# Kernel tuning notes

Measured on AMD Instinct MI355X. Metric: run time of the kernel, lower is better.

## Reference

```python
import jax, jax.numpy as jnp
import numpy as np
from jax.ops import segment_sum, segment_min, segment_max

N, E = 25000, 400000
NF, EF = 30, 10
H = 40          # n_hidden (multiple of towers)
T = 5           # towers
F = H           # F_in per tower (divide_input=False)
FO = H // T     # F_out per tower
L = 2           # gnn layers
NC = 2          # classes
EPS_BN = 1e-5


def setup_inputs() -> dict:
    key = jax.random.key(0)
    ks = jax.random.split(key, 24)
    r = lambda k, s, sc=0.1: jax.random.normal(k, s, jnp.float32) * sc
    return {
        "x": jax.random.normal(ks[0], (N, NF), jnp.float32),
        "edge_attr": jax.random.normal(ks[1], (E, EF), jnp.float32),
        "edge_index": jax.random.randint(ks[2], (2, E), 0, N, jnp.int32),
        "node_w": r(ks[3], (NF, H)), "node_b": r(ks[4], (H,)),
        "edge_w": r(ks[5], (EF, H)), "edge_b": r(ks[6], (H,)),
        "enc_w": r(ks[7], (L, H, F)), "enc_b": r(ks[8], (L, F)),
        "pre_w": r(ks[9], (L, T, 3 * F, F)), "pre_b": r(ks[10], (L, T, F)),
        "post_w": r(ks[11], (L, T, 13 * F, FO)), "post_b": r(ks[12], (L, T, FO)),
        "lin_w": r(ks[13], (L, H, H)), "lin_b": r(ks[14], (L, H)),
        "bn_g": jnp.ones((L, H), jnp.float32), "bn_b": jnp.zeros((L, H), jnp.float32),
        "mlp1_w": r(ks[15], (3 * H, 50)), "mlp1_b": r(ks[16], (50,)),
        "mlp2_w": r(ks[17], (50, 25)), "mlp2_b": r(ks[18], (25,)),
        "mlp3_w": r(ks[19], (25, NC)), "mlp3_b": r(ks[20], (NC,)),
    }


def _pna_conv(x, src, dst, e_emb, enc_w, enc_b, pre_w, pre_b, post_w, post_b,
              lin_w, lin_b, cnt, cnt1, amp, att):
    # message: per-tower pre-MLP on cat(x_i=dst, x_j=src, enc(edge_attr))
    e = e_emb @ enc_w + enc_b                                    # [E, F]
    h = jnp.concatenate([x[dst], x[src], e], axis=-1)            # [E, 3F]
    hs = jnp.einsum('ef,tfo->eto', h, pre_w) + pre_b             # [E, T, F]
    # multi-aggregation over incoming edges (index = dst)
    c = cnt1[:, None, None]
    mean = segment_sum(hs, dst, num_segments=N) / c
    msq = segment_sum(hs * hs, dst, num_segments=N) / c
    std = jnp.sqrt(jax.nn.relu(msq - mean * mean) + 1e-5)
    has = (cnt > 0)[:, None, None]
    mn = jnp.where(has, segment_min(hs, dst, num_segments=N), 0.0)
    mx = jnp.where(has, segment_max(hs, dst, num_segments=N), 0.0)
    agg = jnp.concatenate([mean, mn, mx, std], axis=-1)          # [N, T, 4F]
    agg = jnp.concatenate([agg, agg * amp, agg * att], axis=-1)  # [N, T, 12F]
    out = jnp.concatenate(
        [jnp.broadcast_to(x[:, None, :], (N, T, F)), agg], axis=-1)  # [N, T, 13F]
    out = jnp.einsum('ntf,tfo->nto', out, post_w) + post_b       # [N, T, FO]
    return out.reshape(N, T * FO) @ lin_w + lin_b                # [N, H]


def reference(x, edge_attr, node_w, node_b, edge_w, edge_b, enc_w, enc_b,
              pre_w, pre_b, post_w, post_b, lin_w, lin_b, bn_g, bn_b,
              mlp1_w, mlp1_b, mlp2_w, mlp2_b, mlp3_w, mlp3_b, edge_index):
    src, dst = edge_index[0], edge_index[1]
    cnt = segment_sum(jnp.ones((E,), jnp.float32), dst, num_segments=N)  # in-degree
    cnt1 = jnp.maximum(cnt, 1.0)                                 # deg.clamp_(1)
    log_deg = jnp.log(cnt1 + 1.0)
    avg_log = jnp.mean(jnp.log(cnt + 1.0))                       # PNA avg_deg['log']
    amp = (log_deg / avg_log)[:, None, None]
    att = (avg_log / log_deg)[:, None, None]
    h = x @ node_w + node_b                                      # node embedding
    e_emb = edge_attr @ edge_w + edge_b                          # edge embedding
    for i in range(L):
        c = _pna_conv(h, src, dst, e_emb, enc_w[i], enc_b[i], pre_w[i], pre_b[i],
                      post_w[i], post_b[i], lin_w[i], lin_b[i], cnt, cnt1, amp, att)
        mu = jnp.mean(c, axis=0)
        var = jnp.mean((c - mu) ** 2, axis=0)                    # BatchNorm (batch stats)
        cbn = (c - mu) / jnp.sqrt(var + EPS_BN) * bn_g[i] + bn_b[i]
        h = (h + jax.nn.relu(cbn)) / 2.0
    z = jax.nn.relu(jnp.concatenate([h[src], h[dst]], axis=-1))  # [E, 2H]
    z = jnp.concatenate([z, e_emb], axis=-1)                     # [E, 3H]
    z = jax.nn.relu(z @ mlp1_w + mlp1_b)
    z = jax.nn.relu(z @ mlp2_w + mlp2_b)
    return z @ mlp3_w + mlp3_b                                   # [E, NC]
```

## Files before the change

### kernel.cpp

```cpp
#include <hip/hip_runtime.h>
#include <hip/hip_bf16.h>
#include <cstdint>
#include <cstddef>

#define NN 25000
#define NE 400000
#define NFD 30
#define EFD 10
#define H 40
#define T 5
#define FO 8
#define LAYERS 2
#define TF 200
#define PSTR 52
#define REC 12
#define WCN 416
#define WCK 64
#define SHP 72
#define EPSV 1e-5f

typedef __attribute__((ext_vector_type(8))) short bf16x8;
typedef __attribute__((ext_vector_type(4))) float f32x4;

__device__ inline short bfbits(float v) {
    __hip_bfloat16 b = __float2bfloat16(v);
    return *(short*)&b;
}

__global__ __launch_bounds__(256) void k_deg(const int* __restrict__ dst, int* __restrict__ cnt) {
    int e = blockIdx.x * 256 + threadIdx.x;
    if (e < NE) atomicAdd(&cnt[dst[e]], 1);
}

__global__ __launch_bounds__(256) void k_avglog(const int* __restrict__ cnt, float* __restrict__ slot) {
    __shared__ float red[256];
    float s = 0.0f;
    for (int i = blockIdx.x * 256 + threadIdx.x; i < NN; i += gridDim.x * 256)
        s += logf((float)cnt[i] + 1.0f);
    red[threadIdx.x] = s; __syncthreads();
    for (int o = 128; o > 0; o >>= 1) {
        if (threadIdx.x < o) red[threadIdx.x] += red[threadIdx.x + o];
        __syncthreads();
    }
    if (threadIdx.x == 0) atomicAdd(slot, red[0]);
}

__global__ __launch_bounds__(256) void k_node(const float* __restrict__ x, const float* __restrict__ w,
                                              const float* __restrict__ b, float* __restrict__ h,
                                              const int* __restrict__ cnt, const float* __restrict__ slot,
                                              float* __restrict__ amp, float* __restrict__ att) {
    int id = blockIdx.x * 256 + threadIdx.x;
    if (id < NN) {
        float avg = slot[0] / (float)NN;
        float c1 = fmaxf((float)cnt[id], 1.0f);
        float lg = logf(c1 + 1.0f);
        amp[id] = lg / avg;
        att[id] = avg / lg;
    }
    if (id >= NN * H) return;
    int n = id / H, j = id - n * H;
    const float* xr = x + (size_t)n * NFD;
    float acc = b[j];
    #pragma unroll
    for (int m = 0; m < NFD; m++) acc += xr[m] * w[m * H + j];
    h[id] = acc;
}

__global__ __launch_bounds__(1024) void k_scan(const int* __restrict__ cnt, int* __restrict__ offs) {
    __shared__ int wsum[16];
    int tid = threadIdx.x;
    int lane = tid & 63, wv = tid >> 6;
    int runbase = 0;
    for (int base = 0; base < NN; base += 4096) {
        int i0 = base + tid * 4;
        int4 v = make_int4(0, 0, 0, 0);
        if (i0 < NN) v = *(const int4*)(cnt + i0);
        int tsum = v.x + v.y + v.z + v.w;
        int x = tsum;
        #pragma unroll
        for (int o = 1; o < 64; o <<= 1) {
            int y = __shfl_up(x, o);
            if (lane >= o) x += y;
        }
        if (lane == 63) wsum[wv] = x;
        __syncthreads();
        if (wv == 0 && lane < 16) {
            int wsv = wsum[lane];
            #pragma unroll
            for (int o = 1; o < 16; o <<= 1) {
                int y = __shfl_up(wsv, o);
                if (lane >= o) wsv += y;
            }
            wsum[lane] = wsv;
        }
        __syncthreads();
        int wpref = (wv > 0) ? wsum[wv - 1] : 0;
        int excl = runbase + wpref + x - tsum;
        if (i0 < NN) {
            offs[i0]     = excl;
            offs[i0 + 1] = excl + v.x;
            offs[i0 + 2] = excl + v.x + v.y;
            offs[i0 + 3] = excl + v.x + v.y + v.z;
        }
        runbase += wsum[15];
        __syncthreads();
    }
    if (tid == 0) offs[NN] = runbase;
}

__global__ __launch_bounds__(256) void k_scatter(const int* __restrict__ src, const int* __restrict__ dst,
                                                 const float* __restrict__ edge_attr,
                                                 const int* __restrict__ offs, int* __restrict__ fill,
                                                 float* __restrict__ ea_csr, int* __restrict__ pdst) {
    int e = blockIdx.x * 256 + threadIdx.x;
    if (e >= NE) return;
    int d = dst[e];
    int p = offs[d] + atomicAdd(&fill[d], 1);
    const float2* ear = (const float2*)(edge_attr + (size_t)e * EFD);
    float2 v0 = ear[0], v1 = ear[1], v2 = ear[2], v3 = ear[3], v4 = ear[4];
    float4* o = (float4*)(ea_csr + (size_t)p * REC);
    o[0] = make_float4(v0.x, v0.y, v1.x, v1.y);
    o[1] = make_float4(v2.x, v2.y, v3.x, v3.y);
    o[2] = make_float4(v4.x, v4.y, __int_as_float(src[e]), __int_as_float(e));
    pdst[p] = d;
}

__global__ __launch_bounds__(256) void k_prep1(const float* __restrict__ enc_w, const float* __restrict__ enc_b,
                                               const float* __restrict__ edge_w, const float* __restrict__ edge_b,
                                               const float* __restrict__ pre_w, const float* __restrict__ pre_b,
                                               const float* __restrict__ post_w,
                                               const float* __restrict__ w1, const float* __restrict__ b1,
                                               float* __restrict__ W3e, float* __restrict__ dvecF,
                                               __hip_bfloat16* __restrict__ Wcat,
                                               float* __restrict__ Wp4, float* __restrict__ Wxd,
                                               float* __restrict__ W1e, float* __restrict__ b1e, int layer) {
    int id = blockIdx.x * 256 + threadIdx.x;
    const int B0 = EFD * TF;
    const int B1 = B0 + WCN * WCK;
    const int B2 = B1 + EFD * 50;
    const int B3 = B2 + 40 * 512;
    const int B4 = B3 + H * H;
    if (id < B0) {
        int m = id / TF, j = id - m * TF;
        int t = j / H, f = j - t * H;
        const float* ew = enc_w + (size_t)layer * H * H;
        const float* pw = pre_w + (size_t)(layer * T + t) * 120 * H;
        float acc = 0.0f;
        for (int k = 0; k < H; k++) {
            float wk = edge_w[m * H + k];
            float g = 0.0f;
            #pragma unroll
            for (int o = 0; o < H; o++) g += ew[k * H + o] * pw[(80 + o) * H + f];
            acc += wk * g;
        }
        W3e[m * TF + j] = acc;
        if (m == 0) {
            const float* eb = enc_b + (size_t)layer * H;
            float dacc = pre_b[(size_t)(layer * T + t) * H + f];
            for (int o = 0; o < H; o++) {
                float ebe = eb[o];
                #pragma unroll
                for (int k = 0; k < H; k++) ebe += edge_b[k] * ew[k * H + o];
                dacc += ebe * pw[(80 + o) * H + f];
            }
            dvecF[j] = dacc;
        }
    } else if (id < B1) {
        int id2 = id - B0;
        int j = id2 / WCK, k = id2 - j * WCK;
        float val = 0.0f;
        if (k < H) {
            if (j < TF) {
                int t = j / H, f = j - t * H;
                val = pre_w[((size_t)(layer * T + t) * 120 + k) * H + f];
            } else if (j >= 208 && j < 208 + TF) {
                int j2 = j - 208;
                int t = j2 / H, f = j2 - t * H;
                val = pre_w[((size_t)(layer * T + t) * 120 + H + k) * H + f];
            }
        }
        Wcat[id2] = __float2bfloat16(val);
    } else if (id < B2) {
        if (layer == 0) {
            int id2 = id - B1;
            int m = id2 / 50, o = id2 - m * 50;
            float acc = 0.0f;
            #pragma unroll
            for (int k = 0; k < H; k++) acc += edge_w[m * H + k] * w1[(80 + k) * 50 + o];
            W1e[m * 50 + o] = acc;
            if (m == 0) {
                float bacc = b1[o];
                #pragma unroll
                for (int k = 0; k < H; k++) bacc += edge_b[k] * w1[(80 + k) * 50 + o];
                b1e[o] = bacc;
            }
        }
    } else if (id < B3) {
        int i2 = id - B2;
        int fs4 = i2 >> 9;
        int rem = i2 & 511;
        int col = rem >> 2, c = rem & 3;
        int fs = fs4 * 4 + c;
        float v = 0.0f;
        if (col < 120) {
            int t = col / 24, r2 = col - t * 24;
            int grp = r2 >> 3, o = r2 & 7;
            v = post_w[((size_t)(layer * T + t) * 520 + 40 + grp * 160 + fs) * FO + o];
        }
        Wp4[i2] = v;
    } else if (id < B4) {
        int i2 = id - B3;
        int j = i2 / H, f = i2 - j * H;
        int t = j >> 3, o = j & 7;
        Wxd[i2] = post_w[((size_t)(layer * T + t) * 520 + f) * FO + o];
    }
}

__global__ __launch_bounds__(256) void k_abm(float* h, const float* __restrict__ cbuf,
                                             const float* __restrict__ bnsum, const float* __restrict__ bnsq,
                                             const float* __restrict__ bng, const float* __restrict__ bnb,
                                             int doBN,
                                             const __hip_bfloat16* __restrict__ Wcat,
                                             float* __restrict__ A, __hip_bfloat16* __restrict__ Bbf) {
    __shared__ short sh[64 * SHP];
    int tid = threadIdx.x;
    int n0 = blockIdx.x * 64;
    int nodes = NN - n0; if (nodes > 64) nodes = 64;
    for (int i = tid; i < 64 * SHP; i += 256) sh[i] = 0;
    __syncthreads();
    float invN = 1.0f / (float)NN;
    for (int i = tid; i < nodes * H; i += 256) {
        int f = i % H;
        float hv = h[(size_t)n0 * H + i];
        float hn;
        if (doBN) {
            float mu = bnsum[f] * invN;
            float var = bnsq[f] * invN - mu * mu;
            float c = (cbuf[(size_t)n0 * H + i] - mu) * rsqrtf(var + EPSV) * bng[f] + bnb[f];
            hn = (hv + fmaxf(c, 0.0f)) * 0.5f;
            h[(size_t)n0 * H + i] = hn;
        } else {
            hn = hv;
        }
        sh[(i / H) * SHP + f] = bfbits(hn);
    }
    __syncthreads();

    int wv = tid >> 6, lane = tid & 63;
    int q = lane >> 4, c16 = lane & 15;
    const short* arow = sh + (wv * 16 + c16) * SHP + q * 8;
    bf16x8 a0 = *(const bf16x8*)(arow);
    bf16x8 a1 = *(const bf16x8*)(arow + 32);
    int gm = n0 + wv * 16 + q * 4;

    for (int jt = 0; jt < 26; jt++) {
        int col = jt * 16 + c16;
        const short* wrow = (const short*)Wcat + (size_t)col * WCK + q * 8;
        bf16x8 b0 = *(const bf16x8*)(wrow);
        bf16x8 b1 = *(const bf16x8*)(wrow + 32);
        f32x4 acc = {0.0f, 0.0f, 0.0f, 0.0f};
        acc = __builtin_amdgcn_mfma_f32_16x16x32_bf16(a0, b0, acc, 0, 0, 0);
        acc = __builtin_amdgcn_mfma_f32_16x16x32_bf16(a1, b1, acc, 0, 0, 0);
        if (col < TF) {
            #pragma unroll
            for (int r = 0; r < 4; r++) {
                int row = gm + r;
                if (row < NN) A[(size_t)row * TF + col] = acc[r];
            }
        } else if (col >= 208) {
            int c2 = col - 208;
            if (c2 < TF) {
                #pragma unroll
                for (int r = 0; r < 4; r++) {
                    int row = gm + r;
                    if (row < NN) Bbf[(size_t)row * TF + c2] = __float2bfloat16(acc[r]);
                }
            }
        }
    }
}

__global__ __launch_bounds__(256) void k_agg(const float* __restrict__ ea_csr,
                                             const __hip_bfloat16* __restrict__ Bbf,
                                             const float* __restrict__ A, const float* __restrict__ w3e,
                                             const float* __restrict__ dvecF, const int* __restrict__ cnt,
                                             const int* __restrict__ offs,
                                             const float* __restrict__ h,
                                             const float* __restrict__ Wp4, const float* __restrict__ Wxd,
                                             const float* __restrict__ pbL,
                                             const float* __restrict__ amp, const float* __restrict__ att,
                                             float* __restrict__ cpre) {
    __shared__ float sst[4 * 800];
    __shared__ float shh[4 * H];
    float* spart = sst;
    int tid = threadIdx.x;
    int lane = tid & 63;
    int wv = tid >> 6;
    int n0 = blockIdx.x * 4;
    int n = __builtin_amdgcn_readfirstlane(n0 + wv);
    if (tid < 4 * H) shh[tid] = h[(size_t)n0 * H + tid];
    int deg = cnt[n];
    int start = offs[n];
    bool comp = lane < TF / 4;
    float4 w3q[EFD];
    float4 dj4 = make_float4(0, 0, 0, 0), a4 = make_float4(0, 0, 0, 0);
    if (comp) {
        #pragma unroll
        for (int m = 0; m < EFD; m++) w3q[m] = *(const float4*)(w3e + m * TF + 4 * lane);
        dj4 = *(const float4*)(dvecF + 4 * lane);
        a4  = *(const float4*)(A + (size_t)n * TF + 4 * lane);
    }
    float sx = 0, sy = 0, sz = 0, sw_ = 0;
    float qx = 0, qy = 0, qz = 0, qw = 0;
    float mnx = 3.4e38f, mny = 3.4e38f, mnz = 3.4e38f, mnw = 3.4e38f;
    float mxx = -3.4e38f, mxy = -3.4e38f, mxz = -3.4e38f, mxw = -3.4e38f;
    const float4* recb = (const float4*)ea_csr + (size_t)start * 3;
    const uint16_t* Bu = (const uint16_t*)Bbf;

    auto edge = [&](float4 qa, float4 qb, float4 qc, uint2 bv) {
        float b0 = __uint_as_float(bv.x << 16);
        float b1 = __uint_as_float(bv.x & 0xffff0000u);
        float b2 = __uint_as_float(bv.y << 16);
        float b3 = __uint_as_float(bv.y & 0xffff0000u);
        float eav[EFD] = {qa.x, qa.y, qa.z, qa.w, qb.x, qb.y, qb.z, qb.w, qc.x, qc.y};
        float cx = dj4.x, cy = dj4.y, cz = dj4.z, cw = dj4.w;
        #pragma unroll
        for (int m = 0; m < EFD; m++) {
            cx = fmaf(eav[m], w3q[m].x, cx);
            cy = fmaf(eav[m], w3q[m].y, cy);
            cz = fmaf(eav[m], w3q[m].z, cz);
            cw = fmaf(eav[m], w3q[m].w, cw);
        }
        float ux = b0 + cx, uy = b1 + cy, uz = b2 + cz, uw = b3 + cw;
        sx += ux; qx = fmaf(ux, ux, qx); mnx = fminf(mnx, ux); mxx = fmaxf(mxx, ux);
        sy += uy; qy = fmaf(uy, uy, qy); mny = fminf(mny, uy); mxy = fmaxf(mxy, uy);
        sz += uz; qz = fmaf(uz, uz, qz); mnz = fminf(mnz, uz); mxz = fmaxf(mxz, uz);
        sw_ += uw; qw = fmaf(uw, uw, qw); mnw = fminf(mnw, uw); mxw = fmaxf(mxw, uw);
    };

    int r = 0;
    for (; r + 4 <= deg; r += 4) {
        float4 qa0 = recb[(r + 0) * 3], qb0 = recb[(r + 0) * 3 + 1], qc0 = recb[(r + 0) * 3 + 2];
        float4 qa1 = recb[(r + 1) * 3], qb1 = recb[(r + 1) * 3 + 1], qc1 = recb[(r + 1) * 3 + 2];
        float4 qa2 = recb[(r + 2) * 3], qb2 = recb[(r + 2) * 3 + 1], qc2 = recb[(r + 2) * 3 + 2];
        float4 qa3 = recb[(r + 3) * 3], qb3 = recb[(r + 3) * 3 + 1], qc3 = recb[(r + 3) * 3 + 2];
        int s0 = __float_as_int(qc0.z), s1 = __float_as_int(qc1.z);
        int s2 = __float_as_int(qc2.z), s3 = __float_as_int(qc3.z);
        if (comp) {
            uint2 v0 = *(const uint2*)(Bu + (size_t)s0 * TF + 4 * lane);
            uint2 v1 = *(const uint2*)(Bu + (size_t)s1 * TF + 4 * lane);
            uint2 v2 = *(const uint2*)(Bu + (size_t)s2 * TF + 4 * lane);
            uint2 v3 = *(const uint2*)(Bu + (size_t)s3 * TF + 4 * lane);
            edge(qa0, qb0, qc0, v0);
            edge(qa1, qb1, qc1, v1);
            edge(qa2, qb2, qc2, v2);
            edge(qa3, qb3, qc3, v3);
        }
    }
    for (; r < deg; r++) {
        float4 qa = recb[r * 3], qb = recb[r * 3 + 1], qc = recb[r * 3 + 2];
        int sn = __float_as_int(qc.z);
        if (comp) {
            uint2 bv = *(const uint2*)(Bu + (size_t)sn * TF + 4 * lane);
            edge(qa, qb, qc, bv);
        }
    }
    if (comp) {
        float d = (float)deg, c1 = fmaxf(d, 1.0f);
        float inv = 1.0f / c1;
        float mex = (d * a4.x + sx) * inv, mey = (d * a4.y + sy) * inv;
        float mez = (d * a4.z + sz) * inv, mew = (d * a4.w + sw_) * inv;
        float msx = (d * a4.x * a4.x + 2.0f * a4.x * sx + qx) * inv;
        float msy = (d * a4.y * a4.y + 2.0f * a4.y * sy + qy) * inv;
        float msz = (d * a4.z * a4.z + 2.0f * a4.z * sz + qz) * inv;
        float msw = (d * a4.w * a4.w + 2.0f * a4.w * sw_ + qw) * inv;
        float4 mean4 = make_float4(mex, mey, mez, mew);
        float4 sd4 = make_float4(sqrtf(fmaxf(msx - mex * mex, 0.0f) + EPSV),
                                 sqrtf(fmaxf(msy - mey * mey, 0.0f) + EPSV),
                                 sqrtf(fmaxf(msz - mez * mez, 0.0f) + EPSV),
                                 sqrtf(fmaxf(msw - mew * mew, 0.0f) + EPSV));
        bool has = deg > 0;
        float4 mnv4 = has ? make_float4(a4.x + mnx, a4.y + mny, a4.z + mnz, a4.w + mnw)
                          : make_float4(0, 0, 0, 0);
        float4 mxv4 = has ? make_float4(a4.x + mxx, a4.y + mxy, a4.z + mxz, a4.w + mxw)
                          : make_float4(0, 0, 0, 0);
        int j0 = 4 * lane;
        int t = j0 / H, f = j0 - t * H;
        float* sb = sst + wv * 800 + t * 160 + f;
        *(float4*)(sb)       = mean4;
        *(float4*)(sb + 40)  = mnv4;
        *(float4*)(sb + 80)  = mxv4;
        *(float4*)(sb + 120) = sd4;
    }
    __syncthreads();

    {
        int op = tid & 127, half = tid >> 7;
        int tt = op / 24; if (tt > 4) tt = 4;
        const float* wtp = Wp4 + (size_t)(half * 20) * 512 + op * 4;
        const float* sb0 = sst + tt * 160 + half * 80;
        float p0 = 0, p1 = 0, p2 = 0, p3 = 0;
        #pragma unroll 4
        for (int k = 0; k < 20; k++) {
            float4 w = *(const float4*)(wtp + (size_t)k * 512);
            const float* sp = sb0 + k * 4;
            float4 v0 = *(const float4*)(sp);
            float4 v1 = *(const float4*)(sp + 800);
            float4 v2 = *(const float4*)(sp + 1600);
            float4 v3 = *(const float4*)(sp + 2400);
            p0 += v0.x * w.x + v0.y * w.y + v0.z * w.z + v0.w * w.w;
            p1 += v1.x * w.x + v1.y * w.y + v1.z * w.z + v1.w * w.w;
            p2 += v2.x * w.x + v2.y * w.y + v2.z * w.z + v2.w * w.w;
            p3 += v3.x * w.x + v3.y * w.y + v3.z * w.z + v3.w * w.w;
        }
        __syncthreads();
        if (op < 120) {
            spart[(0 * 120 + op) * 2 + half] = p0;
            spart[(1 * 120 + op) * 2 + half] = p1;
            spart[(2 * 120 + op) * 2 + half] = p2;
            spart[(3 * 120 + op) * 2 + half] = p3;
        }
    }
    __syncthreads();

    if (tid < 160) {
        int nd = tid / H, j = tid - nd * H;
        int t = j >> 3, o = j & 7;
        int ng = n0 + nd;
        float am = amp[ng], at = att[ng];
        const float* yr = spart + (nd * 120 + t * 24) * 2;
        float pa = yr[o * 2]        + yr[o * 2 + 1];
        float pb = yr[(8 + o) * 2]  + yr[(8 + o) * 2 + 1];
        float pc = yr[(16 + o) * 2] + yr[(16 + o) * 2 + 1];
        float acc = pbL[j] + pa + am * pb + at * pc;
        const float* hr = shh + nd * H;
        const float* wx = Wxd + (size_t)j * H;
        #pragma unroll
        for (int fq = 0; fq < 10; fq++) {
            float4 hv = *(const float4*)(hr + fq * 4);
            float4 wv = *(const float4*)(wx + fq * 4);
            acc += hv.x * wv.x + hv.y * wv.y + hv.z * wv.z + hv.w * wv.w;
        }
        cpre[(size_t)ng * H + j] = acc;
    }
}

__global__ __launch_bounds__(256) void k_linbn(const float* __restrict__ cpre, const float* __restrict__ lin_w,
                                               const float* __restrict__ lin_b, float* __restrict__ cbuf,
                                               float* __restrict__ bnsum, float* __restrict__ bnsq, int layer) {
    __shared__ float scp[240];
    __shared__ float red[80];
    int tid = threadIdx.x;
    int j = tid % H, nl = tid / H;
    const float* lw = lin_w + (size_t)layer * H * H;
    float wcol[H];
    #pragma unroll
    for (int k = 0; k < H; k++) wcol[k] = lw[k * H + j];
    float lb = lin_b[(size_t)layer * H + j];
    float lsum = 0.0f, lsq = 0.0f;
    for (int n0 = blockIdx.x * 6; n0 < NN; n0 += gridDim.x * 6) {
        int nn = NN - n0; if (nn > 6) nn = 6;
        if (tid < nn * H) scp[tid] = cpre[(size_t)n0 * H + tid];
        __syncthreads();
        if (nl < nn) {
            float acc = lb;
            #pragma unroll
            for (int k = 0; k < H; k++) acc += scp[nl * H + k] * wcol[k];
            cbuf[(size_t)(n0 + nl) * H + j] = acc;
            lsum += acc; lsq += acc * acc;
        }
        __syncthreads();
    }
    if (tid < 80) red[tid] = 0.0f;
    __syncthreads();
    if (nl < 6) { atomicAdd(&red[j], lsum); atomicAdd(&red[40 + j], lsq); }
    __syncthreads();
    if (tid < 40) atomicAdd(&bnsum[tid], red[tid]);
    else if (tid < 80) atomicAdd(&bnsq[tid - 40], red[tid]);
}

__global__ __launch_bounds__(256) void k_prep2(const float* __restrict__ h, const float* __restrict__ cbuf,
                                               const float* __restrict__ bnsum, const float* __restrict__ bnsq,
                                               const float* __restrict__ bng, const float* __restrict__ bnb,
                                               const float* __restrict__ w1,
                                               float* __restrict__ P1, float* __restrict__ P2) {
    __shared__ float sh[5 * H];
    int tid = threadIdx.x;
    int n0 = blockIdx.x * 5;
    if (tid < 5 * H) {
        int j = tid % H;
        float invN = 1.0f / (float)NN;
        float mu = bnsum[j] * invN;
        float var = bnsq[j] * invN - mu * mu;
        float inv = rsqrtf(var + EPSV);
        float cv = (cbuf[(size_t)n0 * H + tid] - mu) * inv * bng[j] + bnb[j];
        sh[tid] = (h[(size_t)n0 * H + tid] + fmaxf(cv, 0.0f)) * 0.5f;
    }
    __syncthreads();
    if (tid >= 250) return;
    int nl = tid / 50, o = tid - nl * 50;
    const float* hr = sh + nl * H;
    float a1 = 0.0f, a2 = 0.0f;
    #pragma unroll
    for (int f = 0; f < H; f++) {
        float v = fmaxf(hr[f], 0.0f);
        a1 += v * w1[f * 50 + o];
        a2 += v * w1[(H + f) * 50 + o];
    }
    P1[(size_t)(n0 + nl) * PSTR + o] = a1;
    P2[(size_t)(n0 + nl) * PSTR + o] = a2;
}

__global__ __launch_bounds__(256) void k_mlp(const float* __restrict__ ea_csr, const int* __restrict__ pdst,
                                             const float* __restrict__ P1, const float* __restrict__ P2,
                                             const float* __restrict__ W1e, const float* __restrict__ b1e,
                                             const float* __restrict__ w2, const float* __restrict__ b2,
                                             const float* __restrict__ w3, const float* __restrict__ b3,
                                             float* __restrict__ out) {
    int p = blockIdx.x * 256 + threadIdx.x;
    if (p >= NE) return;
    const float4* rec = (const float4*)ea_csr + (size_t)p * 3;
    float4 r0 = rec[0], r1 = rec[1], r2 = rec[2];
    int s = __float_as_int(r2.z), eid = __float_as_int(r2.w);
    int d = pdst[p];
    float ea[EFD] = {r0.x, r0.y, r0.z, r0.w, r1.x, r1.y, r1.z, r1.w, r2.x, r2.y};

    float z1[52];
    const float4* p1r = (const float4*)(P1 + (size_t)s * PSTR);
    const float4* p2r = (const float4*)(P2 + (size_t)d * PSTR);
    #pragma unroll
    for (int i = 0; i < 13; i++) {
        float4 a = p1r[i], b = p2r[i];
        z1[4 * i]     = a.x + b.x;
        z1[4 * i + 1] = a.y + b.y;
        z1[4 * i + 2] = a.z + b.z;
        z1[4 * i + 3] = a.w + b.w;
    }
    #pragma unroll
    for (int k = 0; k < 50; k++) z1[k] += b1e[k];
    #pragma unroll
    for (int m = 0; m < EFD; m++) {
        float v = ea[m];
        #pragma unroll
        for (int k = 0; k < 50; k++) z1[k] = fmaf(v, W1e[m * 50 + k], z1[k]);
    }
    float z2[25];
    #pragma unroll
    for (int o = 0; o < 25; o++) z2[o] = b2[o];
    #pragma unroll
    for (int k = 0; k < 50; k++) {
        float v = fmaxf(z1[k], 0.0f);
        #pragma unroll
        for (int o = 0; o < 25; o++) z2[o] = fmaf(v, w2[k * 25 + o], z2[o]);
    }
    float o0 = b3[0], o1 = b3[1];
    #pragma unroll
    for (int k = 0; k < 25; k++) {
        float v = fmaxf(z2[k], 0.0f);
        o0 = fmaf(v, w3[k * 2], o0);
        o1 = fmaf(v, w3[k * 2 + 1], o1);
    }
    *(float2*)(out + (size_t)eid * 2) = make_float2(o0, o1);
}

extern "C" void kernel_launch(void* const* d_in, const int* in_sizes, int n_in,
                              void* d_out, int out_size, void* d_ws, size_t ws_size,
                              hipStream_t stream) {
    const float* x         = (const float*)d_in[0];
    const float* edge_attr = (const float*)d_in[1];
    const int*   eidx      = (const int*)  d_in[2];
    const float* node_w    = (const float*)d_in[3];
    const float* node_b    = (const float*)d_in[4];
    const float* edge_w    = (const float*)d_in[5];
    const float* edge_b    = (const float*)d_in[6];
    const float* enc_w     = (const float*)d_in[7];
    const float* enc_b     = (const float*)d_in[8];
    const float* pre_w     = (const float*)d_in[9];
    const float* pre_b     = (const float*)d_in[10];
    const float* post_w    = (const float*)d_in[11];
    const float* post_b    = (const float*)d_in[12];
    const float* lin_w     = (const float*)d_in[13];
    const float* lin_b     = (const float*)d_in[14];
    const float* bn_g      = (const float*)d_in[15];
    const float* bn_b      = (const float*)d_in[16];
    const float* w1 = (const float*)d_in[17];
    const float* b1 = (const float*)d_in[18];
    const float* w2 = (const float*)d_in[19];
    const float* b2 = (const float*)d_in[20];
    const float* w3 = (const float*)d_in[21];
    const float* b3 = (const float*)d_in[22];
    const int* srcp = eidx;
    const int* dstp = eidx + NE;
    float* out = (float*)d_out;

    char* ws = (char*)d_ws;
    size_t off = 0;
    auto alloc = [&](size_t bytes) -> char* {
        char* p = ws + off;
        off += (bytes + 255) & ~(size_t)255;
        return p;
    };
    float* h      = (float*)alloc((size_t)NN * H * 4);
    float* Abuf   = (float*)alloc((size_t)NN * TF * 4);
    float* cbuf   = (float*)alloc((size_t)NN * H * 4);
    __hip_bfloat16* Bbf = (__hip_bfloat16*)alloc((size_t)NN * TF * 2 + 256);
    float* cpre   = (float*)alloc((size_t)NN * H * 4);
    float* ea_csr = (float*)alloc((size_t)NE * REC * 4);
    int* pdst     = (int*)alloc((size_t)NE * 4);
    float* W3e    = (float*)alloc((size_t)EFD * TF * 4);
    float* dvecF  = (float*)alloc((size_t)TF * 4);
    __hip_bfloat16* Wcat = (__hip_bfloat16*)alloc((size_t)WCN * WCK * 2);
    float* Wp4    = (float*)alloc((size_t)40 * 512 * 4);
    float* Wxd    = (float*)alloc((size_t)H * H * 4);
    float* P1     = (float*)alloc((size_t)NN * PSTR * 4);
    float* P2     = (float*)alloc((size_t)NN * PSTR * 4);
    float* W1e    = (float*)alloc((size_t)EFD * 50 * 4);
    float* b1e    = (float*)alloc((size_t)64 * 4);
    float* amp    = (float*)alloc((size_t)NN * 4);
    float* att    = (float*)alloc((size_t)NN * 4);
    int* offs     = (int*)alloc((size_t)(NN + 1) * 4);
    size_t zoff = off;
    int* cnt_i    = (int*)alloc((size_t)NN * 4);
    int* fill     = (int*)alloc((size_t)NN * 4);
    float* avgs   = (float*)alloc(256);
    float* bnz    = (float*)alloc(1024);
    size_t zsize = off - zoff;
    if (off > ws_size) return;

    hipMemsetAsync(cnt_i, 0, zsize, stream);

    k_deg<<<(NE + 255) / 256, 256, 0, stream>>>(dstp, cnt_i);
    k_avglog<<<64, 256, 0, stream>>>(cnt_i, avgs);
    k_node<<<(NN * H + 255) / 256, 256, 0, stream>>>(x, node_w, node_b, h, cnt_i, avgs, amp, att);
    k_scan<<<1, 1024, 0, stream>>>(cnt_i, offs);
    k_scatter<<<(NE + 255) / 256, 256, 0, stream>>>(srcp, dstp, edge_attr, offs, fill, ea_csr, pdst);

    int prep1_tot = EFD * TF + WCN * WCK + EFD * 50 + 40 * 512 + H * H;
    int prep1_grid = (prep1_tot + 255) / 256;
    for (int layer = 0; layer < LAYERS; layer++) {
        float* bnzL = bnz + layer * 128;
        k_prep1<<<prep1_grid, 256, 0, stream>>>(
            enc_w, enc_b, edge_w, edge_b, pre_w, pre_b, post_w, w1, b1,
            W3e, dvecF, Wcat, Wp4, Wxd, W1e, b1e, layer);
        float* bnzP = bnz + (layer - 1) * 128;
        k_abm<<<(NN + 63) / 64, 256, 0, stream>>>(
            h, cbuf, (layer > 0) ? bnzP : bnz, (layer > 0) ? bnzP + 40 : bnz,
            bn_g + (size_t)(layer > 0 ? layer - 1 : 0) * H,
            bn_b + (size_t)(layer > 0 ? layer - 1 : 0) * H,
            (layer > 0) ? 1 : 0, Wcat, Abuf, Bbf);
        k_agg<<<NN / 4, 256, 0, stream>>>(ea_csr, Bbf, Abuf, W3e, dvecF, cnt_i, offs,
                                          h, Wp4, Wxd, post_b + (size_t)layer * T * FO,
                                          amp, att, cpre);
        k_linbn<<<1024, 256, 0, stream>>>(cpre, lin_w, lin_b, cbuf, bnzL, bnzL + 40, layer);
    }
    k_prep2<<<NN / 5, 256, 0, stream>>>(h, cbuf, bnz + 128, bnz + 168,
                                        bn_g + H, bn_b + H, w1, P1, P2);
    k_mlp<<<(NE + 255) / 256, 256, 0, stream>>>(ea_csr, pdst, P1, P2, W1e, b1e, w2, b2, w3, b3, out);
}
```

Measured before the change: 571.7 us.

## Fuse linear layer and BN partial stats into aggregation kernel; bf16 post weights

```diff
diff --git a/kernel.cpp b/kernel.cpp
--- a/kernel.cpp
+++ b/kernel.cpp
@@ -17,6 +17,7 @@
 #define WCN 416
 #define WCK 64
 #define SHP 72
+#define NBLK (NN / 4)
 #define EPSV 1e-5f
 
 typedef __attribute__((ext_vector_type(8))) short bf16x8;
@@ -132,7 +133,7 @@
                                                const float* __restrict__ w1, const float* __restrict__ b1,
                                                float* __restrict__ W3e, float* __restrict__ dvecF,
                                                __hip_bfloat16* __restrict__ Wcat,
-                                               float* __restrict__ Wp4, float* __restrict__ Wxd,
+                                               __hip_bfloat16* __restrict__ Wp4b, float* __restrict__ Wxd,
                                                float* __restrict__ W1e, float* __restrict__ b1e, int layer) {
     int id = blockIdx.x * 256 + threadIdx.x;
     const int B0 = EFD * TF;
@@ -207,7 +208,7 @@
             int grp = r2 >> 3, o = r2 & 7;
             v = post_w[((size_t)(layer * T + t) * 520 + 40 + grp * 160 + fs) * FO + o];
         }
-        Wp4[i2] = v;
+        Wp4b[i2] = __float2bfloat16(v);
     } else if (id < B4) {
         int i2 = id - B3;
         int j = i2 / H, f = i2 - j * H;
@@ -286,13 +287,16 @@
                                              const float* __restrict__ dvecF, const int* __restrict__ cnt,
                                              const int* __restrict__ offs,
                                              const float* __restrict__ h,
-                                             const float* __restrict__ Wp4, const float* __restrict__ Wxd,
+                                             const __hip_bfloat16* __restrict__ Wp4b, const float* __restrict__ Wxd,
                                              const float* __restrict__ pbL,
                                              const float* __restrict__ amp, const float* __restrict__ att,
-                                             float* __restrict__ cpre) {
+                                             const float* __restrict__ lwL, const float* __restrict__ lbL,
+                                             float* __restrict__ cbuf, float* __restrict__ partials) {
     __shared__ float sst[4 * 800];
     __shared__ float shh[4 * H];
     float* spart = sst;
+    float* scp   = sst + 1024;
+    float* lred  = sst + 1280;
     int tid = threadIdx.x;
     int lane = tid & 63;
     int wv = tid >> 6;
@@ -397,21 +401,25 @@
     {
         int op = tid & 127, half = tid >> 7;
         int tt = op / 24; if (tt > 4) tt = 4;
-        const float* wtp = Wp4 + (size_t)(half * 20) * 512 + op * 4;
+        const uint16_t* wtp = (const uint16_t*)Wp4b + (size_t)(half * 20) * 512 + op * 4;
         const float* sb0 = sst + tt * 160 + half * 80;
         float p0 = 0, p1 = 0, p2 = 0, p3 = 0;
         #pragma unroll 4
         for (int k = 0; k < 20; k++) {
-            float4 w = *(const float4*)(wtp + (size_t)k * 512);
+            uint2 wb = *(const uint2*)(wtp + (size_t)k * 512);
+            float wx = __uint_as_float(wb.x << 16);
+            float wy = __uint_as_float(wb.x & 0xffff0000u);
+            float wz = __uint_as_float(wb.y << 16);
+            float ww = __uint_as_float(wb.y & 0xffff0000u);
             const float* sp = sb0 + k * 4;
             float4 v0 = *(const float4*)(sp);
             float4 v1 = *(const float4*)(sp + 800);
             float4 v2 = *(const float4*)(sp + 1600);
             float4 v3 = *(const float4*)(sp + 2400);
-            p0 += v0.x * w.x + v0.y * w.y + v0.z * w.z + v0.w * w.w;
-            p1 += v1.x * w.x + v1.y * w.y + v1.z * w.z + v1.w * w.w;
-            p2 += v2.x * w.x + v2.y * w.y + v2.z * w.z + v2.w * w.w;
-            p3 += v3.x * w.x + v3.y * w.y + v3.z * w.z + v3.w * w.w;
+            p0 += v0.x * wx + v0.y * wy + v0.z * wz + v0.w * ww;
+            p1 += v1.x * wx + v1.y * wy + v1.z * wz + v1.w * ww;
+            p2 += v2.x * wx + v2.y * wy + v2.z * wz + v2.w * ww;
+            p3 += v3.x * wx + v3.y * wy + v3.z * wz + v3.w * ww;
         }
         __syncthreads();
         if (op < 120) {
@@ -441,42 +449,44 @@
             float4 wv = *(const float4*)(wx + fq * 4);
             acc += hv.x * wv.x + hv.y * wv.y + hv.z * wv.z + hv.w * wv.w;
         }
-        cpre[(size_t)ng * H + j] = acc;
-    }
-}
-
-__global__ __launch_bounds__(256) void k_linbn(const float* __restrict__ cpre, const float* __restrict__ lin_w,
-                                               const float* __restrict__ lin_b, float* __restrict__ cbuf,
-                                               float* __restrict__ bnsum, float* __restrict__ bnsq, int layer) {
-    __shared__ float scp[240];
-    __shared__ float red[80];
-    int tid = threadIdx.x;
-    int j = tid % H, nl = tid / H;
-    const float* lw = lin_w + (size_t)layer * H * H;
-    float wcol[H];
-    #pragma unroll
-    for (int k = 0; k < H; k++) wcol[k] = lw[k * H + j];
-    float lb = lin_b[(size_t)layer * H + j];
-    float lsum = 0.0f, lsq = 0.0f;
-    for (int n0 = blockIdx.x * 6; n0 < NN; n0 += gridDim.x * 6) {
-        int nn = NN - n0; if (nn > 6) nn = 6;
-        if (tid < nn * H) scp[tid] = cpre[(size_t)n0 * H + tid];
+        scp[tid] = acc;
+    }
+    __syncthreads();
+
+    if (tid < 160) {
+        int nd = tid / H, j = tid - nd * H;
+        const float* scr = scp + nd * H;
+        float lacc = lbL[j];
+        #pragma unroll
+        for (int k = 0; k < H; k++) lacc = fmaf(scr[k], lwL[k * H + j], lacc);
+        cbuf[(size_t)(n0 + nd) * H + j] = lacc;
+        lred[tid] = lacc;
+    }
+    __syncthreads();
+
+    if (tid < 80) {
+        int c2 = tid / 40, j = tid - c2 * 40;
+        float s = 0.0f;
+        #pragma unroll
+        for (int nd = 0; nd < 4; nd++) {
+            float v = lred[nd * 40 + j];
+            s += c2 ? v * v : v;
+        }
+        partials[(size_t)blockIdx.x * 80 + tid] = s;
+    }
+}
+
+__global__ __launch_bounds__(256) void k_bnred(const float* __restrict__ partials, float* __restrict__ dst) {
+    __shared__ float red[256];
+    int b = blockIdx.x;
+    float s = 0.0f;
+    for (int i = threadIdx.x; i < NBLK; i += 256) s += partials[(size_t)i * 80 + b];
+    red[threadIdx.x] = s; __syncthreads();
+    for (int o = 128; o > 0; o >>= 1) {
+        if (threadIdx.x < o) red[threadIdx.x] += red[threadIdx.x + o];
         __syncthreads();
-        if (nl < nn) {
-            float acc = lb;
-            #pragma unroll
-            for (int k = 0; k < H; k++) acc += scp[nl * H + k] * wcol[k];
-            cbuf[(size_t)(n0 + nl) * H + j] = acc;
-            lsum += acc; lsq += acc * acc;
-        }
-        __syncthreads();
-    }
-    if (tid < 80) red[tid] = 0.0f;
-    __syncthreads();
-    if (nl < 6) { atomicAdd(&red[j], lsum); atomicAdd(&red[40 + j], lsq); }
-    __syncthreads();
-    if (tid < 40) atomicAdd(&bnsum[tid], red[tid]);
-    else if (tid < 80) atomicAdd(&bnsq[tid - 40], red[tid]);
+    }
+    if (threadIdx.x == 0) dst[b] = red[0];
 }
 
 __global__ __launch_bounds__(256) void k_prep2(const float* __restrict__ h, const float* __restrict__ cbuf,
@@ -604,13 +614,13 @@
     float* Abuf   = (float*)alloc((size_t)NN * TF * 4);
     float* cbuf   = (float*)alloc((size_t)NN * H * 4);
     __hip_bfloat16* Bbf = (__hip_bfloat16*)alloc((size_t)NN * TF * 2 + 256);
-    float* cpre   = (float*)alloc((size_t)NN * H * 4);
+    float* partials = (float*)alloc((size_t)NBLK * 80 * 4);
     float* ea_csr = (float*)alloc((size_t)NE * REC * 4);
     int* pdst     = (int*)alloc((size_t)NE * 4);
     float* W3e    = (float*)alloc((size_t)EFD * TF * 4);
     float* dvecF  = (float*)alloc((size_t)TF * 4);
     __hip_bfloat16* Wcat = (__hip_bfloat16*)alloc((size_t)WCN * WCK * 2);
-    float* Wp4    = (float*)alloc((size_t)40 * 512 * 4);
+    __hip_bfloat16* Wp4b = (__hip_bfloat16*)alloc((size_t)40 * 512 * 2);
     float* Wxd    = (float*)alloc((size_t)H * H * 4);
     float* P1     = (float*)alloc((size_t)NN * PSTR * 4);
     float* P2     = (float*)alloc((size_t)NN * PSTR * 4);
@@ -641,17 +651,19 @@
         float* bnzL = bnz + layer * 128;
         k_prep1<<<prep1_grid, 256, 0, stream>>>(
             enc_w, enc_b, edge_w, edge_b, pre_w, pre_b, post_w, w1, b1,
-            W3e, dvecF, Wcat, Wp4, Wxd, W1e, b1e, layer);
+            W3e, dvecF, Wcat, Wp4b, Wxd, W1e, b1e, layer);
         float* bnzP = bnz + (layer - 1) * 128;
         k_abm<<<(NN + 63) / 64, 256, 0, stream>>>(
             h, cbuf, (layer > 0) ? bnzP : bnz, (layer > 0) ? bnzP + 40 : bnz,
             bn_g + (size_t)(layer > 0 ? layer - 1 : 0) * H,
             bn_b + (size_t)(layer > 0 ? layer - 1 : 0) * H,
             (layer > 0) ? 1 : 0, Wcat, Abuf, Bbf);
-        k_agg<<<NN / 4, 256, 0, stream>>>(ea_csr, Bbf, Abuf, W3e, dvecF, cnt_i, offs,
-                                          h, Wp4, Wxd, post_b + (size_t)layer * T * FO,
-                                          amp, att, cpre);
-        k_linbn<<<1024, 256, 0, stream>>>(cpre, lin_w, lin_b, cbuf, bnzL, bnzL + 40, layer);
+        k_agg<<<NBLK, 256, 0, stream>>>(ea_csr, Bbf, Abuf, W3e, dvecF, cnt_i, offs,
+                                        h, Wp4b, Wxd, post_b + (size_t)layer * T * FO,
+                                        amp, att,
+                                        lin_w + (size_t)layer * H * H, lin_b + (size_t)layer * H,
+                                        cbuf, partials);
+        k_bnred<<<80, 256, 0, stream>>>(partials, bnzL);
     }
     k_prep2<<<NN / 5, 256, 0, stream>>>(h, cbuf, bnz + 128, bnz + 168,
                                         bn_g + H, bn_b + H, w1, P1, P2);
```

Measured after the change: 537.5 us. 1.06x faster.
